# Kernel tuning notes

Measured on AMD Instinct MI355X. Metric: run time of the kernel, lower is better.

## Reference

```python
import jax, jax.numpy as jnp
import numpy as np


def conv2d(x, w, b=None, pad=0):
    # x: [B,C,H,W], w: [O,I,kh,kw]
    out = jax.lax.conv_general_dilated(
        x, w, window_strides=(1, 1), padding=[(pad, pad), (pad, pad)],
        dimension_numbers=('NCHW', 'OIHW', 'NCHW'))
    if b is not None:
        out = out + b[None, :, None, None]
    return out


def setup_inputs() -> dict:
    key = jax.random.key(0)
    ks = jax.random.split(key, 10)
    B, C, W, H, N, G = 8, 256, 64, 64, 1024, 32
    s = jnp.float32(0.02)  # small init so softmax is not saturated
    return {
        'input_graph': jax.random.normal(ks[0], (B, N, G), jnp.float32),
        'input_image': jax.random.normal(ks[1], (B, C, W, H), jnp.float32),
        'Wq': jax.random.normal(ks[2], (C, C), jnp.float32) * s,
        'bq': jnp.zeros((C,), jnp.float32),
        'Wk': jax.random.normal(ks[3], (C, G), jnp.float32) * s,
        'bk': jnp.zeros((C,), jnp.float32),
        'Wv': jax.random.normal(ks[4], (C, G), jnp.float32) * s,
        'bv': jnp.zeros((C,), jnp.float32),
        'conv1_w': jax.random.normal(ks[5], (C, C, 1, 1), jnp.float32) * s,
        'bn_gamma': jnp.ones((C,), jnp.float32),
        'bn_beta': jnp.zeros((C,), jnp.float32),
        'bn_mean': jnp.zeros((C,), jnp.float32),
        'bn_var': jnp.ones((C,), jnp.float32),
        'conv2_w': jax.random.normal(ks[6], (C, C, 3, 3), jnp.float32) * s,
        'conv2_b': jnp.zeros((C,), jnp.float32),
        'conv3_w': jax.random.normal(ks[7], (C, C, 1, 1), jnp.float32) * s,
        'conv3_b': jnp.zeros((C,), jnp.float32),
    }


def reference(input_graph, input_image, Wq, bq, Wk, bk, Wv, bv,
              conv1_w, bn_gamma, bn_beta, bn_mean, bn_var,
              conv2_w, conv2_b, conv3_w, conv3_b):
    B, C, W, H = input_image.shape
    P = W * H
    g = jnp.transpose(input_graph, (0, 2, 1))  # [B,G,N]
    # 1x1 conv1d projections == per-position matmuls
    K = jnp.einsum('og,bgn->bon', Wk, g) + bk[None, :, None]   # [B,C,N]
    V = jnp.einsum('og,bgn->bon', Wv, g) + bv[None, :, None]   # [B,C,N]
    x = input_image.reshape(B, C, P)
    Q = jnp.einsum('oc,bcp->bop', Wq, x) + bq[None, :, None]   # [B,C,P]
    # att[b,p,n] = sum_c Q[b,c,p] * K[b,c,n]  (Q was permuted to [B,P,C] in torch)
    att = jnp.einsum('bcp,bcn->bpn', Q, K) / jnp.sqrt(jnp.float32(C))
    # NOTE: original applies Softmax(dim=1) -> over the P (pixel) axis
    att = jax.nn.softmax(att, axis=1)
    # message = V @ att^T : [B,C,N] x [B,N,P] -> [B,C,P]
    msg = jnp.einsum('bcn,bpn->bcp', V, att).reshape(B, C, W, H)
    # Conv_Bn_Activation: 1x1 conv (no bias) + BN (inference) + LeakyReLU(0.1)
    h = conv2d(msg, conv1_w)
    inv = jax.lax.rsqrt(bn_var + jnp.float32(1e-5))
    h = (h - bn_mean[None, :, None, None]) * (bn_gamma * inv)[None, :, None, None] + bn_beta[None, :, None, None]
    h = jnp.where(h > 0, h, jnp.float32(0.1) * h)
    h = conv2d(h, conv2_w, conv2_b, pad=1)  # 3x3, pad 1
    return input_image + conv2d(h, conv3_w, conv3_b)  # 1x1
```

## Files before the change

### kernel.cpp

```cpp
#include <hip/hip_runtime.h>
#include <hip/hip_bf16.h>

typedef __hip_bfloat16 bf16;
typedef unsigned short u16;
typedef __attribute__((ext_vector_type(8))) short  b8v;
typedef __attribute__((ext_vector_type(8))) unsigned short u16x8;
typedef __attribute__((ext_vector_type(4))) unsigned short u16x4;
typedef __attribute__((ext_vector_type(4))) float f32x4;

static __device__ __forceinline__ float us2f(u16 s) {
    unsigned int u = ((unsigned int)s) << 16;
    return __builtin_bit_cast(float, u);
}
static __device__ __forceinline__ u16 f2us(float x) {
    union { bf16 h; u16 s; } v; v.h = __float2bfloat16(x); return v.s;
}
static __device__ __forceinline__ float b2f(bf16 x) { return __bfloat162float(x); }
static __device__ __forceinline__ bf16 f2b(float x) { return __float2bfloat16(x); }
static __device__ __forceinline__ float toF(float x) { return x; }
static __device__ __forceinline__ float toF(bf16 x)  { return b2f(x); }
static __device__ __forceinline__ void stor(float* p, float v) { *p = v; }
static __device__ __forceinline__ void stor(bf16* p,  float v) { *p = f2b(v); }

static __device__ __forceinline__ void gload16(const u16* g, u16* l) {
    __builtin_amdgcn_global_load_lds(
        (const __attribute__((address_space(1))) unsigned int*)g,
        (__attribute__((address_space(3))) unsigned int*)l,
        16, 0, 0);
}


__global__ __launch_bounds__(256) void cast_f2b4(const float* __restrict__ src,
                                                 u16* __restrict__ dst, int n4)
{
    int i = blockIdx.x * 256 + threadIdx.x;
    if (i < n4) {
        float4 v = ((const float4*)src)[i];
        u16x4 o = { f2us(v.x), f2us(v.y), f2us(v.z), f2us(v.w) };
        ((u16x4*)dst)[i] = o;
    }
}

__global__ __launch_bounds__(256) void repack_w2(const float* __restrict__ src,
                                                 u16* __restrict__ dst)
{
    int idx = blockIdx.x * 256 + threadIdx.x;
    int o = idx / 2304, k = idx - o * 2304;
    int tap = k >> 8, c = k & 255;
    dst[idx] = f2us(src[(o * 256 + c) * 9 + tap]);
}

__global__ __launch_bounds__(256) void transpose_cast_x(const float* __restrict__ x,
                                                        u16* __restrict__ xT, int C, int P)
{
    __shared__ u16 t[64][72];
    const int b = blockIdx.z, c0 = blockIdx.y * 64, p0 = blockIdx.x * 64;
    const int tid = threadIdx.x;
    const int r = tid >> 2, q = tid & 3;
    const float* src = x + ((size_t)b * C + c0 + r) * P + p0 + q * 16;
#pragma unroll
    for (int i = 0; i < 16; i++) t[q * 16 + i][r] = f2us(src[i]);
    __syncthreads();
    u16* dst = xT + ((size_t)b * P + p0 + r) * C + c0 + q * 16;
    *(u16x8*)dst       = *(u16x8*)&t[r][q * 16];
    *(u16x8*)(dst + 8) = *(u16x8*)&t[r][q * 16 + 8];
}

template<int EPI, typename TA, typename TB, typename TC>
__global__ __launch_bounds__(256) void gemm_any(
    const TA* __restrict__ A, const TB* __restrict__ B, TC* __restrict__ C,
    int M, int Nn, int Kd,
    long saM, long saK, long aB,
    long sbK, long sbN, long bB,
    long scM, long scN, long cB,
    float scale, const float* __restrict__ bias)
{
    __shared__ float As[16][65];
    __shared__ float Bs[16][65];
    const int b  = blockIdx.z;
    const TA* Ab = A + (long)b * aB;
    const TB* Bb = B + (long)b * bB;
    const int m0 = blockIdx.y * 64, n0 = blockIdx.x * 64;
    const int tid = threadIdx.x;
    const int tx = tid & 15, ty = tid >> 4;
    const bool kfA = (saK == 1);
    const bool nfB = (sbN == 1);
    float acc[4][4] = {};

    for (int k0 = 0; k0 < Kd; k0 += 16) {
#pragma unroll
        for (int i = 0; i < 4; i++) {
            int idx = tid + i * 256; int mm, kk;
            if (kfA) { kk = idx & 15; mm = idx >> 4; }
            else     { mm = idx & 63; kk = idx >> 6; }
            As[kk][mm] = toF(Ab[(long)(m0 + mm) * saM + (long)(k0 + kk) * saK]);
        }
#pragma unroll
        for (int i = 0; i < 4; i++) {
            int idx = tid + i * 256; int nn, kk;
            if (nfB) { nn = idx & 63; kk = idx >> 6; }
            else     { kk = idx & 15; nn = idx >> 4; }
            Bs[kk][nn] = toF(Bb[(long)(k0 + kk) * sbK + (long)(n0 + nn) * sbN]);
        }
        __syncthreads();
#pragma unroll
        for (int kk = 0; kk < 16; kk++) {
            float a[4], bb[4];
#pragma unroll
            for (int i = 0; i < 4; i++) a[i]  = As[kk][ty * 4 + i];
#pragma unroll
            for (int j = 0; j < 4; j++) bb[j] = Bs[kk][tx * 4 + j];
#pragma unroll
            for (int i = 0; i < 4; i++)
#pragma unroll
                for (int j = 0; j < 4; j++) acc[i][j] += a[i] * bb[j];
        }
        __syncthreads();
    }
#pragma unroll
    for (int i = 0; i < 4; i++) {
        int m = m0 + ty * 4 + i;
        float add0 = (EPI == 0 && bias) ? bias[m] : 0.f;
#pragma unroll
        for (int j = 0; j < 4; j++) {
            int n = n0 + tx * 4 + j;
            float v = acc[i][j] * scale + add0;
            if (EPI == 3 && bias) v += bias[n];
            stor(&C[(long)b * cB + (long)m * scM + (long)n * scN], v);
        }
    }
}

template<int EPI, bool CT, typename TC, int NTILE>
__global__ __launch_bounds__(256) void gemm_mfma(
    const u16* __restrict__ A, const u16* __restrict__ Bt, TC* __restrict__ Cc,
    int M, int N, int K, int lda, int ldb, int ldc,
    long aBat, long bBat, long cBat,
    float scale, const float* __restrict__ bias,
    const float* __restrict__ gamma, const float* __restrict__ beta,
    const float* __restrict__ mean,  const float* __restrict__ var,
    const float* __restrict__ resid, long rBat, int ldr,
    float* __restrict__ csum)
{
    constexpr int NI = NTILE / 32;
    __shared__ u16 Al[128 * 32];
    __shared__ u16 Bl[NTILE * 32];
    __shared__ float red[2][2][4][16];
    const int bat = blockIdx.z;
    const int m0 = blockIdx.y * 128, n0 = blockIdx.x * NTILE;
    const int tid = threadIdx.x;
    const int lane = tid & 63, wid = tid >> 6;
    const int wr = wid >> 1, wc = wid & 1;
    const int fr = lane & 15, fq = lane >> 4;
    const int sc = ((lane & 3) ^ ((lane >> 3) & 3)) * 8;
    const int axs = (fq ^ ((fr >> 1) & 3)) * 8;

    const u16* gA = A  + (size_t)bat * aBat + (size_t)(m0 + wid * 32 + (lane >> 2)) * lda + sc;
    const u16* gB = Bt + (size_t)bat * bBat + (size_t)(n0 + wid * (NTILE / 4) + (lane >> 2)) * ldb + sc;
    u16* lA = &Al[(wid * 32) * 32];
    u16* lB = &Bl[(wid * (NTILE / 4)) * 32];
    const size_t a16 = (size_t)16 * lda, b16 = (size_t)16 * ldb;

    f32x4 acc[4][NI];
#pragma unroll
    for (int i = 0; i < 4; i++)
#pragma unroll
        for (int j = 0; j < NI; j++) acc[i][j] = (f32x4){0.f, 0.f, 0.f, 0.f};

    for (int k0 = 0; k0 < K; k0 += 32) {
        gload16(gA + k0,       lA);
        gload16(gA + k0 + a16, lA + 16 * 32);
        gload16(gB + k0,       lB);
        if constexpr (NTILE == 128) gload16(gB + k0 + b16, lB + 16 * 32);
        __syncthreads();
        b8v a[4], b[NI];
#pragma unroll
        for (int mi = 0; mi < 4; mi++) a[mi] = *(const b8v*)&Al[(wr * 64 + mi * 16 + fr) * 32 + axs];
#pragma unroll
        for (int ni = 0; ni < NI; ni++) b[ni] = *(const b8v*)&Bl[(wc * (NTILE / 2) + ni * 16 + fr) * 32 + axs];
#pragma unroll
        for (int mi = 0; mi < 4; mi++)
#pragma unroll
            for (int ni = 0; ni < NI; ni++)
                acc[mi][ni] = __builtin_amdgcn_mfma_f32_16x16x32_bf16(a[mi], b[ni], acc[mi][ni], 0, 0, 0);
        __syncthreads();
    }

    const int mbase = m0 + wr * 64, nbase = n0 + wc * (NTILE / 2);
    float cs[NI];
#pragma unroll
    for (int ni = 0; ni < NI; ni++) cs[ni] = 0.f;
#pragma unroll
    for (int mi = 0; mi < 4; mi++) {
        float esc[4], ead[4];
#pragma unroll
        for (int j = 0; j < 4; j++) {
            int m = mbase + mi * 16 + fq * 4 + j;
            if (EPI == 1) {
                float sc2 = gamma[m] * rsqrtf(var[m] + 1e-5f);
                esc[j] = sc2; ead[j] = beta[m] - mean[m] * sc2;
            } else {
                esc[j] = scale; ead[j] = (EPI != 3 && bias) ? bias[m] : 0.f;
            }
        }
#pragma unroll
        for (int ni = 0; ni < NI; ni++) {
            f32x4 v = acc[mi][ni];
            const int n = nbase + ni * 16 + fr;
            if (CT) {
                const int mb = mbase + mi * 16 + fq * 4;
                u16x4 pk;
#pragma unroll
                for (int j = 0; j < 4; j++) {
                    float x = v[j] * esc[j] + ead[j];
                    if (EPI == 1) x = x > 0.f ? x : 0.1f * x;
                    pk[j] = f2us(x);
                }
                *(u16x4*)((u16*)Cc + (size_t)bat * cBat + (size_t)n * ldc + mb) = pk;
            } else {
#pragma unroll
                for (int j = 0; j < 4; j++) {
                    int m = mbase + mi * 16 + fq * 4 + j;
                    float x;
                    if (EPI == 3) { x = __expf(v[j] * esc[j]); cs[ni] += x; }
                    else {
                        x = v[j] * esc[j] + ead[j];
                        if (EPI == 1) x = x > 0.f ? x : 0.1f * x;
                        if (EPI == 2) x += resid[(size_t)bat * rBat + (size_t)m * ldr + n];
                    }
                    TC* p = Cc + (size_t)bat * cBat + (size_t)m * ldc + n;
                    if constexpr (sizeof(TC) == 2) *(u16*)p = f2us(x); else *(float*)p = x;
                }
            }
        }
    }
    if constexpr (EPI == 3) {
#pragma unroll
        for (int ni = 0; ni < NI; ni++) {
            float s = cs[ni];
            s += __shfl_xor(s, 16, 64);
            s += __shfl_xor(s, 32, 64);
            if (fq == 0) red[wr][wc][ni][fr] = s;
        }
        __syncthreads();
        if (tid < NTILE) {
            const int wcc = tid >> 6, nii = (tid >> 4) & 3, frr = tid & 15;
            float s = red[0][wcc][nii][frr] + red[1][wcc][nii][frr];
            csum[((size_t)bat * gridDim.y + blockIdx.y) * ldc + n0 + tid] = s;
        }
    }
}

__global__ __launch_bounds__(256) void conv3x3_mfma(
    const u16* __restrict__ Wt, const u16* __restrict__ X, u16* __restrict__ Y,
    const float* __restrict__ bias)
{
    const int C = 256, P = 4096, K = 2304;
    __shared__ u16 Al[2][128 * 32];
    __shared__ u16 Bl[2][64 * 32];
    const int bat = blockIdx.z;
    const int m0 = blockIdx.y * 128, n0 = blockIdx.x * 64;
    const int y0 = blockIdx.x;
    const int tid = threadIdx.x;
    const int lane = tid & 63, wid = tid >> 6;
    const int wr = wid >> 1, wc = wid & 1;
    const int fr = lane & 15, fq = lane >> 4;
    const int bx = tid & 63, cg = tid >> 6;
    const int scA = ((lane & 3) ^ ((lane >> 3) & 3)) * 8;
    const int axs = (fq ^ ((fr >> 1) & 3)) * 8;
    const int bf = (bx >> 1) & 3;
    const int bc0 = (cg & 1) * 2;

    const u16* Ag = Wt + (size_t)(m0 + wid * 32 + (lane >> 2)) * K + scA;
    u16* lA0 = &Al[0][(wid * 32) * 32];
    u16* lA1 = &Al[1][(wid * 32) * 32];
    const u16* Xb = X + (size_t)bat * C * P;

    f32x4 acc[4][2];
#pragma unroll
    for (int i = 0; i < 4; i++)
#pragma unroll
        for (int j = 0; j < 2; j++) acc[i][j] = (f32x4){0.f, 0.f, 0.f, 0.f};

    u16x8 breg[2];
    auto loadB = [&](int k0) {
        const int tap = k0 >> 8;
        const int c0k = (k0 & 255) + cg * 16;
        const int dy = tap / 3 - 1, dxv = tap - (tap / 3) * 3 - 1;
        const int y = y0 + dy, xs = bx + dxv;
        const bool ok = ((unsigned)y < 64u) && ((unsigned)xs < 64u);
        const int off = ok ? (y * 64 + xs) : 0;
#pragma unroll
        for (int g = 0; g < 2; g++) {
            const u16* src = Xb + (size_t)(c0k + g * 8) * P + off;
            u16x8 v;
#pragma unroll
            for (int l = 0; l < 8; l++) v[l] = src[(size_t)l * P];
            if (!ok) v = (u16x8){0, 0, 0, 0, 0, 0, 0, 0};
            breg[g] = v;
        }
    };

    loadB(0);

    for (int k0 = 0; k0 < K; k0 += 64) {
        gload16(Ag + k0,                       lA0);
        gload16(Ag + k0 + (size_t)16 * K,      lA0 + 16 * 32);
        gload16(Ag + k0 + 32,                  lA1);
        gload16(Ag + k0 + 32 + (size_t)16 * K, lA1 + 16 * 32);
        *(u16x8*)&Bl[cg >> 1][bx * 32 + (bc0 ^ bf) * 8]       = breg[0];
        *(u16x8*)&Bl[cg >> 1][bx * 32 + ((bc0 + 1) ^ bf) * 8] = breg[1];
        __syncthreads();
        if (k0 + 64 < K) loadB(k0 + 64);
#pragma unroll
        for (int t = 0; t < 2; t++) {
            b8v a[4], b[2];
#pragma unroll
            for (int mi = 0; mi < 4; mi++) a[mi] = *(const b8v*)&Al[t][(wr * 64 + mi * 16 + fr) * 32 + axs];
#pragma unroll
            for (int ni = 0; ni < 2; ni++) b[ni] = *(const b8v*)&Bl[t][(wc * 32 + ni * 16 + fr) * 32 + axs];
#pragma unroll
            for (int mi = 0; mi < 4; mi++)
#pragma unroll
                for (int ni = 0; ni < 2; ni++)
                    acc[mi][ni] = __builtin_amdgcn_mfma_f32_16x16x32_bf16(a[mi], b[ni], acc[mi][ni], 0, 0, 0);
        }
        __syncthreads();
    }

    const int mbase = m0 + wr * 64, nbase = n0 + wc * 32;
#pragma unroll
    for (int mi = 0; mi < 4; mi++) {
        const int mb = mbase + mi * 16 + fq * 4;
        float bb[4];
#pragma unroll
        for (int j = 0; j < 4; j++) bb[j] = bias[mb + j];
#pragma unroll
        for (int ni = 0; ni < 2; ni++) {
            const int n = nbase + ni * 16 + fr;
            u16x4 pk;
#pragma unroll
            for (int j = 0; j < 4; j++) pk[j] = f2us(acc[mi][ni][j] + bb[j]);
            *(u16x4*)&Y[(size_t)bat * P * C + (size_t)n * C + mb] = pk;
        }
    }
}

__global__ __launch_bounds__(256) void colsum_merge(const float* __restrict__ part,
                                                    float* __restrict__ sinv, int N, int PC)
{
    const int n = blockIdx.x * 256 + threadIdx.x, b = blockIdx.y;
    const float* pc = part + (size_t)b * PC * N + n;
    float s = 0.f;
    for (int c = 0; c < PC; c++) s += pc[(size_t)c * N];
    sinv[(size_t)b * N + n] = 1.f / s;
}

__global__ __launch_bounds__(256) void scale_v(u16* __restrict__ V,
                                               const float* __restrict__ sinv,
                                               int C, int N)
{
    const size_t base = ((size_t)blockIdx.x * 256 + threadIdx.x) * 8;
    const int n0 = (int)(base % N);
    const int b = (int)(base / ((size_t)C * N));
    const float* sv = sinv + (size_t)b * N + n0;
    u16x8 v = *(u16x8*)&V[base];
#pragma unroll
    for (int j = 0; j < 8; j++) v[j] = f2us(us2f(v[j]) * sv[j]);
    *(u16x8*)&V[base] = v;
}


extern "C" void kernel_launch(void* const* d_in, const int* in_sizes, int n_in,
                              void* d_out, int out_size, void* d_ws, size_t ws_size,
                              hipStream_t stream)
{
    const float* graph = (const float*)d_in[0];
    const float* image = (const float*)d_in[1];
    const float* Wq  = (const float*)d_in[2];
    const float* bq  = (const float*)d_in[3];
    const float* Wk  = (const float*)d_in[4];
    const float* bk  = (const float*)d_in[5];
    const float* Wv  = (const float*)d_in[6];
    const float* bv  = (const float*)d_in[7];
    const float* c1w = (const float*)d_in[8];
    const float* gam = (const float*)d_in[9];
    const float* bet = (const float*)d_in[10];
    const float* mea = (const float*)d_in[11];
    const float* var = (const float*)d_in[12];
    const float* c2w = (const float*)d_in[13];
    const float* c2b = (const float*)d_in[14];
    const float* c3w = (const float*)d_in[15];
    const float* c3b = (const float*)d_in[16];
    float* out = (float*)d_out;

    const int B = 8, C = 256, P = 4096, N = 1024, G = 32;
    const size_t MiB = 1024 * 1024, KiB = 1024;
    char* ws = (char*)d_ws;
    u16* E     = (u16*)(ws);
    u16* xT    = (u16*)(ws);
    u16* Wq_b  = (u16*)(ws + 16 * MiB);
    u16* Qt    = (u16*)(ws + 64 * MiB);
    u16* msgT  = Qt;
    float* sinv = (float*)(ws + 80 * MiB);
    u16* c1w_b = (u16*)(ws + 80 * MiB + 64 * KiB);
    u16* c3w_b = (u16*)(ws + 80 * MiB + 192 * KiB);
    u16* c2w_b = (u16*)(ws + 80 * MiB + 320 * KiB);
    u16* Kt    = (u16*)(ws + 80 * MiB);
    u16* Vb    = (u16*)(ws + 84 * MiB);
    u16* h1    = (u16*)(ws);
    u16* h2T   = (u16*)(ws + 16 * MiB);
    float* part = out;

    transpose_cast_x<<<dim3(P / 64, C / 64, B), 256, 0, stream>>>(image, xT, C, P);
    cast_f2b4<<<64,  256, 0, stream>>>(Wq,  Wq_b,  16384);
    gemm_any<3, float, float, bf16><<<dim3(C / 64, N / 64, B), 256, 0, stream>>>(
        graph, Wk, (bf16*)Kt, N, C, G,
        G, 1, (long)N * G,   1, G, 0,   C, 1, (long)N * C, 1.f, bk);
    gemm_any<0, float, float, bf16><<<dim3(N / 64, C / 64, B), 256, 0, stream>>>(
        Wv, graph, (bf16*)Vb, C, N, G,
        G, 1, 0,   1, G, (long)N * G,   N, 1, (long)C * N, 1.f, bv);

    gemm_mfma<0, true, u16, 64><<<dim3(P / 64, C / 128, B), 256, 0, stream>>>(
        Wq_b, xT, Qt, C, P, C, C, C, C,
        0, (long)P * C, (long)P * C, 1.f, bq,
        nullptr, nullptr, nullptr, nullptr, nullptr, 0, 0, nullptr);
    gemm_mfma<3, false, u16, 128><<<dim3(N / 128, P / 128, B), 256, 0, stream>>>(
        Qt, Kt, E, P, N, C, C, C, N,
        (long)P * C, (long)N * C, (long)P * N, 0.0625f, nullptr,
        nullptr, nullptr, nullptr, nullptr, nullptr, 0, 0, part);
    cast_f2b4<<<64,   256, 0, stream>>>(c1w, c1w_b, 16384);
    cast_f2b4<<<64,   256, 0, stream>>>(c3w, c3w_b, 16384);
    repack_w2<<<2304, 256, 0, stream>>>(c2w, c2w_b);
    colsum_merge<<<dim3(N / 256, B), 256, 0, stream>>>(part, sinv, N, P / 128);
    scale_v<<<dim3((int)((size_t)B * C * N / 8 / 256)), 256, 0, stream>>>(Vb, sinv, C, N);
    gemm_mfma<0, true, u16, 64><<<dim3(P / 64, C / 128, B), 256, 0, stream>>>(
        Vb, E, msgT, C, P, N, N, N, C,
        (long)C * N, (long)P * N, (long)P * C, 1.f, nullptr,
        nullptr, nullptr, nullptr, nullptr, nullptr, 0, 0, nullptr);
    gemm_mfma<1, false, u16, 64><<<dim3(P / 64, C / 128, B), 256, 0, stream>>>(
        c1w_b, msgT, h1, C, P, C, C, C, P,
        0, (long)P * C, (long)C * P, 1.f, nullptr,
        gam, bet, mea, var, nullptr, 0, 0, nullptr);
    conv3x3_mfma<<<dim3(P / 64, C / 128, B), 256, 0, stream>>>(c2w_b, h1, h2T, c2b);
    gemm_mfma<2, false, float, 64><<<dim3(P / 64, C / 128, B), 256, 0, stream>>>(
        c3w_b, h2T, out, C, P, C, C, C, P,
        0, (long)P * C, (long)C * P, 1.f, c3b,
        nullptr, nullptr, nullptr, nullptr, image, (long)C * P, P, nullptr);
}
```

Before: 231.2 us.

## Reassociate Q and conv1 projections into K and V, pad conv input

Folds Wq into K (KW = K·Wq, plus a per-column bias term tq from bq) so the attention logits come straight from the image, with no full Q projection over all pixels. Folds conv1 into V (VV = conv1·V scaled by the softmax inverse sums), so the message GEMM emits the BN+LeakyReLU activations directly and the separate conv1 GEMM over P disappears. The conv3x3 input is now written into a zero-halo padded channel-last layout, so B tiles load with async gload16 and swizzled LDS instead of bounds-checked strided scalar loads, at the cost of dropping the register prefetch of B. Scratch buffers are moved into the output buffer, and the different rounding order in bf16 may change numerics slightly.

```diff
diff --git a/kernel.cpp b/kernel.cpp
--- a/kernel.cpp
+++ b/kernel.cpp
@@ -209,6 +209,7 @@
             const int n = nbase + ni * 16 + fr;
             if (CT) {
                 const int mb = mbase + mi * 16 + fq * 4;
+                const int prow = ((n >> 6) + 1) * 66 + (n & 63) + 1;
                 u16x4 pk;
 #pragma unroll
                 for (int j = 0; j < 4; j++) {
@@ -216,14 +217,16 @@
                     if (EPI == 1) x = x > 0.f ? x : 0.1f * x;
                     pk[j] = f2us(x);
                 }
-                *(u16x4*)((u16*)Cc + (size_t)bat * cBat + (size_t)n * ldc + mb) = pk;
+                *(u16x4*)((u16*)Cc + (size_t)bat * cBat + (size_t)prow * ldc + mb) = pk;
             } else {
 #pragma unroll
                 for (int j = 0; j < 4; j++) {
                     int m = mbase + mi * 16 + fq * 4 + j;
                     float x;
-                    if (EPI == 3) { x = __expf(v[j] * esc[j]); cs[ni] += x; }
-                    else {
+                    if (EPI == 3) {
+                        x = __expf((v[j] + (bias ? bias[(size_t)bat * N + n] : 0.f)) * esc[j]);
+                        cs[ni] += x;
+                    } else {
                         x = v[j] * esc[j] + ead[j];
                         if (EPI == 1) x = x > 0.f ? x : 0.1f * x;
                         if (EPI == 2) x += resid[(size_t)bat * rBat + (size_t)m * ldr + n];
@@ -252,29 +255,28 @@
 }
 
 __global__ __launch_bounds__(256) void conv3x3_mfma(
-    const u16* __restrict__ Wt, const u16* __restrict__ X, u16* __restrict__ Y,
+    const u16* __restrict__ Wt, const u16* __restrict__ Xp, u16* __restrict__ Y,
     const float* __restrict__ bias)
 {
     const int C = 256, P = 4096, K = 2304;
     __shared__ u16 Al[2][128 * 32];
-    __shared__ u16 Bl[2][64 * 32];
+    __shared__ u16 Bl[64 * 64];
     const int bat = blockIdx.z;
-    const int m0 = blockIdx.y * 128, n0 = blockIdx.x * 64;
+    const int m0 = blockIdx.y * 128;
     const int y0 = blockIdx.x;
     const int tid = threadIdx.x;
     const int lane = tid & 63, wid = tid >> 6;
     const int wr = wid >> 1, wc = wid & 1;
     const int fr = lane & 15, fq = lane >> 4;
-    const int bx = tid & 63, cg = tid >> 6;
     const int scA = ((lane & 3) ^ ((lane >> 3) & 3)) * 8;
     const int axs = (fq ^ ((fr >> 1) & 3)) * 8;
-    const int bf = (bx >> 1) & 3;
-    const int bc0 = (cg & 1) * 2;
 
     const u16* Ag = Wt + (size_t)(m0 + wid * 32 + (lane >> 2)) * K + scA;
     u16* lA0 = &Al[0][(wid * 32) * 32];
     u16* lA1 = &Al[1][(wid * 32) * 32];
-    const u16* Xb = X + (size_t)bat * C * P;
+    const u16* Xb = Xp + (size_t)bat * 66 * 66 * 256;
+
+    const int brow = (lane >> 3), bq = lane & 7;
 
     f32x4 acc[4][2];
 #pragma unroll
@@ -282,43 +284,34 @@
 #pragma unroll
         for (int j = 0; j < 2; j++) acc[i][j] = (f32x4){0.f, 0.f, 0.f, 0.f};
 
-    u16x8 breg[2];
-    auto loadB = [&](int k0) {
-        const int tap = k0 >> 8;
-        const int c0k = (k0 & 255) + cg * 16;
+    for (int k0 = 0; k0 < K; k0 += 64) {
+        const int tap = k0 >> 8, c0k = k0 & 255;
         const int dy = tap / 3 - 1, dxv = tap - (tap / 3) * 3 - 1;
-        const int y = y0 + dy, xs = bx + dxv;
-        const bool ok = ((unsigned)y < 64u) && ((unsigned)xs < 64u);
-        const int off = ok ? (y * 64 + xs) : 0;
-#pragma unroll
-        for (int g = 0; g < 2; g++) {
-            const u16* src = Xb + (size_t)(c0k + g * 8) * P + off;
-            u16x8 v;
-#pragma unroll
-            for (int l = 0; l < 8; l++) v[l] = src[(size_t)l * P];
-            if (!ok) v = (u16x8){0, 0, 0, 0, 0, 0, 0, 0};
-            breg[g] = v;
-        }
-    };
-
-    loadB(0);
-
-    for (int k0 = 0; k0 < K; k0 += 64) {
+        const int syp = y0 + dy + 1;
         gload16(Ag + k0,                       lA0);
         gload16(Ag + k0 + (size_t)16 * K,      lA0 + 16 * 32);
         gload16(Ag + k0 + 32,                  lA1);
         gload16(Ag + k0 + 32 + (size_t)16 * K, lA1 + 16 * 32);
-        *(u16x8*)&Bl[cg >> 1][bx * 32 + (bc0 ^ bf) * 8]       = breg[0];
-        *(u16x8*)&Bl[cg >> 1][bx * 32 + ((bc0 + 1) ^ bf) * 8] = breg[1];
-        __syncthreads();
-        if (k0 + 64 < K) loadB(k0 + 64);
+#pragma unroll
+        for (int h = 0; h < 2; h++) {
+            const int g = wid * 2 + h;
+            const int r = g * 8 + brow;
+            const int qs = bq ^ (r & 7);
+            const u16* src = Xb + ((size_t)syp * 66 + (r + dxv + 1)) * 256 + c0k + qs * 8;
+            gload16(src, &Bl[g * 512]);
+        }
+        __syncthreads();
 #pragma unroll
         for (int t = 0; t < 2; t++) {
             b8v a[4], b[2];
 #pragma unroll
             for (int mi = 0; mi < 4; mi++) a[mi] = *(const b8v*)&Al[t][(wr * 64 + mi * 16 + fr) * 32 + axs];
 #pragma unroll
-            for (int ni = 0; ni < 2; ni++) b[ni] = *(const b8v*)&Bl[t][(wc * 32 + ni * 16 + fr) * 32 + axs];
+            for (int ni = 0; ni < 2; ni++) {
+                const int row = wc * 32 + ni * 16 + fr;
+                const int ch = ((t * 4 + fq) ^ (fr & 7)) * 8;
+                b[ni] = *(const b8v*)&Bl[row * 64 + ch];
+            }
 #pragma unroll
             for (int mi = 0; mi < 4; mi++)
 #pragma unroll
@@ -328,7 +321,7 @@
         __syncthreads();
     }
 
-    const int mbase = m0 + wr * 64, nbase = n0 + wc * 32;
+    const int mbase = m0 + wr * 64, nbase = y0 * 64 + wc * 32;
 #pragma unroll
     for (int mi = 0; mi < 4; mi++) {
         const int mb = mbase + mi * 16 + fq * 4;
@@ -344,6 +337,22 @@
             *(u16x4*)&Y[(size_t)bat * P * C + (size_t)n * C + mb] = pk;
         }
     }
+}
+
+
+__global__ __launch_bounds__(256) void tq_dot(const u16* __restrict__ Kt,
+                                              const float* __restrict__ bq,
+                                              float* __restrict__ tq, int N, int C)
+{
+    const int n = blockIdx.x * 256 + threadIdx.x, b = blockIdx.y;
+    const u16* row = Kt + ((size_t)b * N + n) * C;
+    float s = 0.f;
+    for (int c = 0; c < C; c += 8) {
+        u16x8 v = *(const u16x8*)&row[c];
+#pragma unroll
+        for (int j = 0; j < 8; j++) s += us2f(v[j]) * bq[c + j];
+    }
+    tq[(size_t)b * N + n] = s;
 }
 
 __global__ __launch_bounds__(256) void colsum_merge(const float* __restrict__ part,
@@ -356,18 +365,33 @@
     sinv[(size_t)b * N + n] = 1.f / s;
 }
 
-__global__ __launch_bounds__(256) void scale_v(u16* __restrict__ V,
-                                               const float* __restrict__ sinv,
-                                               int C, int N)
+__global__ __launch_bounds__(256) void scale_vt(u16* __restrict__ Vt,
+                                                const float* __restrict__ sinv,
+                                                int N, int C)
 {
     const size_t base = ((size_t)blockIdx.x * 256 + threadIdx.x) * 8;
-    const int n0 = (int)(base % N);
-    const int b = (int)(base / ((size_t)C * N));
-    const float* sv = sinv + (size_t)b * N + n0;
-    u16x8 v = *(u16x8*)&V[base];
-#pragma unroll
-    for (int j = 0; j < 8; j++) v[j] = f2us(us2f(v[j]) * sv[j]);
-    *(u16x8*)&V[base] = v;
+    const int n = (int)((base / C) % N);
+    const int b = (int)(base / ((size_t)N * C));
+    const float s = sinv[(size_t)b * N + n];
+    u16x8 v = *(u16x8*)&Vt[base];
+#pragma unroll
+    for (int j = 0; j < 8; j++) v[j] = f2us(us2f(v[j]) * s);
+    *(u16x8*)&Vt[base] = v;
+}
+
+__global__ __launch_bounds__(256) void zero_halo(u16* __restrict__ Xp)
+{
+    int i = blockIdx.x * 256 + threadIdx.x;
+    const int ch8 = i & 31; i >>= 5;
+    const int hp = i % 260;
+    const int b = i / 260;
+    int py, px;
+    if (hp < 66)       { py = 0;  px = hp; }
+    else if (hp < 132) { py = 65; px = hp - 66; }
+    else if (hp < 196) { py = hp - 132 + 1; px = 0; }
+    else               { py = hp - 196 + 1; px = 65; }
+    u16x8 z = {0, 0, 0, 0, 0, 0, 0, 0};
+    *(u16x8*)&Xp[(((size_t)b * 66 + py) * 66 + px) * 256 + ch8 * 8] = z;
 }
 
 
@@ -397,52 +421,55 @@
     const int B = 8, C = 256, P = 4096, N = 1024, G = 32;
     const size_t MiB = 1024 * 1024, KiB = 1024;
     char* ws = (char*)d_ws;
-    u16* E     = (u16*)(ws);
-    u16* xT    = (u16*)(ws);
-    u16* Wq_b  = (u16*)(ws + 16 * MiB);
-    u16* Qt    = (u16*)(ws + 64 * MiB);
-    u16* msgT  = Qt;
-    float* sinv = (float*)(ws + 80 * MiB);
-    u16* c1w_b = (u16*)(ws + 80 * MiB + 64 * KiB);
-    u16* c3w_b = (u16*)(ws + 80 * MiB + 192 * KiB);
-    u16* c2w_b = (u16*)(ws + 80 * MiB + 320 * KiB);
-    u16* Kt    = (u16*)(ws + 80 * MiB);
-    u16* Vb    = (u16*)(ws + 84 * MiB);
-    u16* h1    = (u16*)(ws);
-    u16* h2T   = (u16*)(ws + 16 * MiB);
-    float* part = out;
+    char* dob = (char*)d_out;
+    u16* WqT  = (u16*)(ws);
+    u16* E    = (u16*)(ws);
+    u16* xT   = (u16*)(ws + 64 * MiB);
+    u16* Kt   = (u16*)(ws + 80 * MiB);
+    u16* VV   = (u16*)(ws + 80 * MiB);
+    u16* Vt   = (u16*)(ws + 84 * MiB);
+    u16* h2T  = (u16*)(ws);
+    u16* c2w_b = (u16*)(ws + 17 * MiB);
+    u16* c3w_b = (u16*)(ws + 19 * MiB);
+    float* part = (float*)(dob);
+    u16* KWt   = (u16*)(dob + 2 * MiB);
+    float* tqb = (float*)(dob + 6 * MiB);
+    float* sinv = (float*)(dob + 7 * MiB);
+    u16* c1w_b = (u16*)(dob + 8 * MiB);
+    u16* h1p   = (u16*)(dob + 14 * MiB);
 
     transpose_cast_x<<<dim3(P / 64, C / 64, B), 256, 0, stream>>>(image, xT, C, P);
-    cast_f2b4<<<64,  256, 0, stream>>>(Wq,  Wq_b,  16384);
+    transpose_cast_x<<<dim3(4, 4, 1), 256, 0, stream>>>(Wq, WqT, 256, 256);
+    cast_f2b4<<<64, 256, 0, stream>>>(c1w, c1w_b, 16384);
     gemm_any<3, float, float, bf16><<<dim3(C / 64, N / 64, B), 256, 0, stream>>>(
         graph, Wk, (bf16*)Kt, N, C, G,
         G, 1, (long)N * G,   1, G, 0,   C, 1, (long)N * C, 1.f, bk);
-    gemm_any<0, float, float, bf16><<<dim3(N / 64, C / 64, B), 256, 0, stream>>>(
-        Wv, graph, (bf16*)Vb, C, N, G,
-        G, 1, 0,   1, G, (long)N * G,   N, 1, (long)C * N, 1.f, bv);
-
-    gemm_mfma<0, true, u16, 64><<<dim3(P / 64, C / 128, B), 256, 0, stream>>>(
-        Wq_b, xT, Qt, C, P, C, C, C, C,
-        0, (long)P * C, (long)P * C, 1.f, bq,
+    gemm_any<3, float, float, bf16><<<dim3(C / 64, N / 64, B), 256, 0, stream>>>(
+        graph, Wv, (bf16*)Vt, N, C, G,
+        G, 1, (long)N * G,   1, G, 0,   C, 1, (long)N * C, 1.f, bv);
+    gemm_mfma<0, false, u16, 64><<<dim3(C / 64, N / 128, B), 256, 0, stream>>>(
+        Kt, WqT, KWt, N, C, C, C, C, C,
+        (long)N * C, 0, (long)N * C, 1.f, nullptr,
         nullptr, nullptr, nullptr, nullptr, nullptr, 0, 0, nullptr);
+    tq_dot<<<dim3(N / 256, B), 256, 0, stream>>>(Kt, bq, tqb, N, C);
     gemm_mfma<3, false, u16, 128><<<dim3(N / 128, P / 128, B), 256, 0, stream>>>(
-        Qt, Kt, E, P, N, C, C, C, N,
-        (long)P * C, (long)N * C, (long)P * N, 0.0625f, nullptr,
+        xT, KWt, E, P, N, C, C, C, N,
+        (long)P * C, (long)N * C, (long)P * N, 0.0625f, tqb,
         nullptr, nullptr, nullptr, nullptr, nullptr, 0, 0, part);
-    cast_f2b4<<<64,   256, 0, stream>>>(c1w, c1w_b, 16384);
-    cast_f2b4<<<64,   256, 0, stream>>>(c3w, c3w_b, 16384);
+    colsum_merge<<<dim3(N / 256, B), 256, 0, stream>>>(part, sinv, N, P / 128);
+    scale_vt<<<dim3((int)((size_t)B * N * C / 8 / 256)), 256, 0, stream>>>(Vt, sinv, N, C);
+    gemm_mfma<0, false, u16, 64><<<dim3(N / 64, C / 128, B), 256, 0, stream>>>(
+        c1w_b, Vt, VV, C, N, C, C, C, N,
+        0, (long)N * C, (long)C * N, 1.f, nullptr,
+        nullptr, nullptr, nullptr, nullptr, nullptr, 0, 0, nullptr);
+    gemm_mfma<1, true, u16, 64><<<dim3(P / 64, C / 128, B), 256, 0, stream>>>(
+        VV, E, h1p, C, P, N, N, N, C,
+        (long)C * N, (long)P * N, (long)66 * 66 * C, 1.f, nullptr,
+        gam, bet, mea, var, nullptr, 0, 0, nullptr);
+    zero_halo<<<260, 256, 0, stream>>>(h1p);
     repack_w2<<<2304, 256, 0, stream>>>(c2w, c2w_b);
-    colsum_merge<<<dim3(N / 256, B), 256, 0, stream>>>(part, sinv, N, P / 128);
-    scale_v<<<dim3((int)((size_t)B * C * N / 8 / 256)), 256, 0, stream>>>(Vb, sinv, C, N);
-    gemm_mfma<0, true, u16, 64><<<dim3(P / 64, C / 128, B), 256, 0, stream>>>(
-        Vb, E, msgT, C, P, N, N, N, C,
-        (long)C * N, (long)P * N, (long)P * C, 1.f, nullptr,
-        nullptr, nullptr, nullptr, nullptr, nullptr, 0, 0, nullptr);
-    gemm_mfma<1, false, u16, 64><<<dim3(P / 64, C / 128, B), 256, 0, stream>>>(
-        c1w_b, msgT, h1, C, P, C, C, C, P,
-        0, (long)P * C, (long)C * P, 1.f, nullptr,
-        gam, bet, mea, var, nullptr, 0, 0, nullptr);
-    conv3x3_mfma<<<dim3(P / 64, C / 128, B), 256, 0, stream>>>(c2w_b, h1, h2T, c2b);
+    cast_f2b4<<<64, 256, 0, stream>>>(c3w, c3w_b, 16384);
+    conv3x3_mfma<<<dim3(P / 64, C / 128, B), 256, 0, stream>>>(c2w_b, h1p, h2T, c2b);
     gemm_mfma<2, false, float, 64><<<dim3(P / 64, C / 128, B), 256, 0, stream>>>(
         c3w_b, h2T, out, C, P, C, C, C, P,
         0, (long)P * C, (long)C * P, 1.f, c3b,
```

After: 238.7 us. 1.03x slower.
